# Optimization experiments

Hardware: AMD Instinct MI355X
Metric: run time of the kernel (lower is better)

The kernel has to match this reference:

```python
import jax, jax.numpy as jnp
import numpy as np

B, T, E = 32, 512, 256
H = 512          # num_cells
REV_H = 10       # hardcoded LSTM(10)
CONV_C = 60      # hardcoded Conv1D(60)
FEAT = 3 * CONV_C + REV_H  # 190
D0 = 100
TEMP = 1e-5
EPS = 1e-20


def setup_inputs() -> dict:
    key = jax.random.key(0)
    ks = jax.random.split(key, 18)
    def g(k, shape, fan_in):
        return (jax.random.normal(k, shape, jnp.float32) / np.float32(np.sqrt(fan_in)))
    inp = {}
    inp["x"] = jax.random.normal(ks[0], (B, T, E), jnp.float32)
    # Conv1D kernels in WIO layout [k, in, out]
    inp["conv1_w"] = g(ks[1], (3, E, CONV_C), 3 * E)
    inp["conv1_b"] = jnp.zeros((CONV_C,), jnp.float32)
    inp["conv2_w"] = g(ks[2], (4, E, CONV_C), 4 * E)
    inp["conv2_b"] = jnp.zeros((CONV_C,), jnp.float32)
    inp["conv3_w"] = g(ks[3], (5, E, CONV_C), 5 * E)
    inp["conv3_b"] = jnp.zeros((CONV_C,), jnp.float32)
    # reverse LSTM(10)
    inp["rev_Wx"] = g(ks[4], (E, 4 * REV_H), E)
    inp["rev_Wh"] = g(ks[5], (REV_H, 4 * REV_H), REV_H)
    inp["rev_b"] = jnp.zeros((4 * REV_H,), jnp.float32)
    # gate MLP: Dense(100, relu) -> Dense(2)
    inp["d0_W"] = g(ks[6], (FEAT + E, D0), FEAT + E)
    inp["d0_b"] = jnp.zeros((D0,), jnp.float32)
    inp["d1_W"] = g(ks[7], (D0, 2), D0)
    inp["d1_b"] = jnp.zeros((2,), jnp.float32)
    # main LSTMCell(H)
    inp["cell_Wx"] = g(ks[8], (E, 4 * H), E)
    inp["cell_Wh"] = g(ks[9], (H, 4 * H), H)
    inp["cell_b"] = jnp.zeros((4 * H,), jnp.float32)
    # pre-sampled Gumbel(0,1) noise, one per (t, b, 2)
    U = jax.random.uniform(ks[10], (T, B, 2), jnp.float32, 1e-7, 1.0)
    inp["gumbel_noise"] = -jnp.log(-jnp.log(U + EPS) + EPS)
    return inp


def _lstm_scan(xseq, Wx, Wh, b):
    # xseq: [T, B, E] -> hs: [T, B, H]
    h_dim = Wh.shape[0]
    bsz = xseq.shape[1]
    def step(carry, xt):
        h, c = carry
        z = xt @ Wx + h @ Wh + b
        i, f, g_, o = jnp.split(z, 4, axis=-1)
        c = jax.nn.sigmoid(f) * c + jax.nn.sigmoid(i) * jnp.tanh(g_)
        h = jax.nn.sigmoid(o) * jnp.tanh(c)
        return (h, c), h
    init = (jnp.zeros((bsz, h_dim), xseq.dtype), jnp.zeros((bsz, h_dim), xseq.dtype))
    _, hs = jax.lax.scan(step, init, xseq)
    return hs


def reference(x, conv1_w, conv1_b, conv2_w, conv2_b, conv3_w, conv3_b,
              rev_Wx, rev_Wh, rev_b, d0_W, d0_b, d1_W, d1_b,
              cell_Wx, cell_Wh, cell_b, gumbel_noise):
    dn = ('NWC', 'WIO', 'NWC')
    def conv(w, b_):
        return jax.lax.conv_general_dilated(x, w, (1,), 'SAME', dimension_numbers=dn) + b_
    conved = jnp.concatenate([conv(conv1_w, conv1_b), conv(conv2_w, conv2_b), conv(conv3_w, conv3_b)], axis=-1)  # [B,T,180]
    # LSTM over reversed sequence (output NOT re-reversed, as in the original)
    x_rev = x[:, ::-1, :].transpose(1, 0, 2)               # [T,B,E]
    rev = _lstm_scan(x_rev, rev_Wx, rev_Wh, rev_b).transpose(1, 0, 2)  # [B,T,10]
    f_core = jnp.concatenate([conved, rev], axis=-1)        # [B,T,190]
    # f_all[:, t+1] for t in [0,T): shift left by one, pad a zero row at the end
    ff_seq = jnp.concatenate([f_core[:, 1:, :], jnp.zeros_like(f_core[:, :1, :])], axis=1)  # [B,T,190]

    bsz = x.shape[0]
    h_dim = cell_Wh.shape[0]
    xs = (x.transpose(1, 0, 2), ff_seq.transpose(1, 0, 2), gumbel_noise)

    def step(carry, inputs):
        h, c = carry
        xt, ff, gn = inputs
        # skip-gate logits -> Gumbel-softmax (temperature 1e-5)
        hid = jax.nn.relu(jnp.concatenate([ff, xt], axis=-1) @ d0_W + d0_b)
        pi = hid @ d1_W + d1_b                               # [B,2]
        d = jax.nn.softmax((pi + gn) / TEMP, axis=-1)        # [B,2]
        # LSTM cell candidate
        z = xt @ cell_Wx + h @ cell_Wh + cell_b
        i, f, g_, o = jnp.split(z, 4, axis=-1)
        c_cand = jax.nn.sigmoid(f) * c + jax.nn.sigmoid(i) * jnp.tanh(g_)
        h_cand = jax.nn.sigmoid(o) * jnp.tanh(c_cand)
        d0, d1 = d[:, :1], d[:, 1:]
        h_new = d0 * h_cand + d1 * h
        c_new = d0 * c_cand + d1 * c
        # output written each step is the (ungated) candidate h, per the source
        return (h_new, c_new), h_cand

    init = (jnp.zeros((bsz, h_dim), x.dtype), jnp.zeros((bsz, h_dim), x.dtype))
    _, outs = jax.lax.scan(step, init, xs)                  # [T,B,H]
    return outs.transpose(1, 0, 2)                          # [B,T,H]
```

## Files before the change

kernel.cpp:

```cpp
#include <hip/hip_runtime.h>
#include <math.h>

#define Bz 32
#define Tz 512
#define Ez 256
#define Hz 512
#define FCH 446

__device__ __forceinline__ float sigf(float x){ return 1.0f/(1.0f + __expf(-x)); }
__device__ __forceinline__ float tanhfast(float x){ return 1.0f - 2.0f/(__expf(2.0f*x) + 1.0f); }

__global__ __launch_bounds__(256) void k_transpose_wh(const float* __restrict__ Wh, float* __restrict__ WhT){
  int idx = blockIdx.x*256 + threadIdx.x;
  int k = idx >> 11, c = idx & 2047;
  WhT[c*512 + k] = Wh[idx];
}

__global__ __launch_bounds__(256) void k_conv(
    const float* __restrict__ x,
    const float* __restrict__ w1, const float* __restrict__ b1,
    const float* __restrict__ w2, const float* __restrict__ b2,
    const float* __restrict__ w3, const float* __restrict__ b3,
    const float* __restrict__ rwx,
    float* __restrict__ feat, float* __restrict__ rxw)
{
  __shared__ __align__(16) float xs[256*40];
  int b  = blockIdx.x >> 4;
  int t0 = (blockIdx.x & 15) * 32;
  int tid = threadIdx.x;
  for (int i = 0; i < 36; ++i){
    int t = t0 - 2 + i;
    xs[tid*40 + i] = (t >= 0 && t < Tz) ? x[(b*Tz + t)*Ez + tid] : 0.0f;
  }
  __syncthreads();
  for (int i = 0; i < 32; ++i){
    int t = t0 + i;
    feat[((size_t)t*Bz + b)*FCH + 190 + tid] = xs[tid*40 + i + 2];
  }
  int tq = tid & 7, cs = tid >> 3;
  float acc[6][4];
  float racc[2][4];
  #pragma unroll
  for (int ci = 0; ci < 6; ++ci){
    int c = cs + 32*ci;
    float bv = 0.0f;
    if (c < 60) bv = b1[c];
    else if (c < 120) bv = b2[c-60];
    else if (c < 180) bv = b3[c-120];
    acc[ci][0]=acc[ci][1]=acc[ci][2]=acc[ci][3]=bv;
  }
  #pragma unroll
  for (int ji = 0; ji < 2; ++ji){ racc[ji][0]=racc[ji][1]=racc[ji][2]=racc[ji][3]=0.0f; }

  for (int e = 0; e < 256; ++e){
    const float* xr = &xs[e*40 + 4*tq];
    float4 wa = *(const float4*)(xr);
    float4 wb = *(const float4*)(xr + 4);
    float wd[8] = {wa.x, wa.y, wa.z, wa.w, wb.x, wb.y, wb.z, wb.w};
    #pragma unroll
    for (int ci = 0; ci < 6; ++ci){
      int c = cs + 32*ci;
      if (c < 60){
        #pragma unroll
        for (int k = 0; k < 3; ++k){
          float wv = w1[(k*256 + e)*60 + c];
          #pragma unroll
          for (int j = 0; j < 4; ++j) acc[ci][j] = fmaf(wd[1 + j + k], wv, acc[ci][j]);
        }
      } else if (c < 120){
        int cc = c - 60;
        #pragma unroll
        for (int k = 0; k < 4; ++k){
          float wv = w2[(k*256 + e)*60 + cc];
          #pragma unroll
          for (int j = 0; j < 4; ++j) acc[ci][j] = fmaf(wd[1 + j + k], wv, acc[ci][j]);
        }
      } else if (c < 180){
        int cc = c - 120;
        #pragma unroll
        for (int k = 0; k < 5; ++k){
          float wv = w3[(k*256 + e)*60 + cc];
          #pragma unroll
          for (int j = 0; j < 4; ++j) acc[ci][j] = fmaf(wd[j + k], wv, acc[ci][j]);
        }
      }
    }
    #pragma unroll
    for (int ji = 0; ji < 2; ++ji){
      int jc = cs + 32*ji;
      if (jc < 40){
        float wv = rwx[e*40 + jc];
        #pragma unroll
        for (int j = 0; j < 4; ++j) racc[ji][j] = fmaf(wd[2 + j], wv, racc[ji][j]);
      }
    }
  }
  #pragma unroll
  for (int ci = 0; ci < 6; ++ci){
    int c = cs + 32*ci;
    if (c < 180){
      #pragma unroll
      for (int j = 0; j < 4; ++j){
        int t = t0 + 4*tq + j;
        if (t >= 1) feat[((size_t)(t-1)*Bz + b)*FCH + c] = acc[ci][j];
      }
    }
  }
  #pragma unroll
  for (int ji = 0; ji < 2; ++ji){
    int jc = cs + 32*ji;
    if (jc < 40){
      #pragma unroll
      for (int j = 0; j < 4; ++j){
        int t = t0 + 4*tq + j;
        rxw[((size_t)(511 - t)*Bz + b)*40 + jc] = racc[ji][j];
      }
    }
  }
}

__global__ __launch_bounds__(64) void k_rev(const float* __restrict__ rxw,
    const float* __restrict__ revWh, const float* __restrict__ revb, float* __restrict__ feat){
  int b = blockIdx.x;
  int j = threadIdx.x;
  float wreg[10];
  float bias = 0.0f;
  #pragma unroll
  for (int k = 0; k < 10; ++k) wreg[k] = 0.0f;
  if (j < 40){
    bias = revb[j];
    #pragma unroll
    for (int k = 0; k < 10; ++k) wreg[k] = revWh[k*40 + j];
  }
  float h[10];
  #pragma unroll
  for (int k = 0; k < 10; ++k) h[k] = 0.0f;
  float c = 0.0f;
  for (int s = 0; s < Tz; ++s){
    float z = bias + ((j < 40) ? rxw[(s*Bz + b)*40 + j] : 0.0f);
    #pragma unroll
    for (int k = 0; k < 10; ++k) z = fmaf(h[k], wreg[k], z);
    float a = (j >= 20 && j < 30) ? tanhfast(z) : sigf(z);
    float af = __shfl(a, j + 10);
    float ag = __shfl(a, j + 20);
    float ao = __shfl(a, j + 30);
    if (j < 10) c = af*c + a*ag;
    float hn = ao * tanhfast(c);
    #pragma unroll
    for (int k = 0; k < 10; ++k) h[k] = __shfl(hn, k);
    if (j < 10 && s >= 1) feat[((size_t)(s-1)*Bz + b)*FCH + 180 + j] = hn;
  }
}

__global__ __launch_bounds__(256) void k_hid(const float* __restrict__ feat,
    const float* __restrict__ d0W, const float* __restrict__ d0b, float* __restrict__ hid){
  __shared__ __align__(16) float fT[446*36];
  int r0 = blockIdx.x * 32;
  int tid = threadIdx.x;
  for (int r = 0; r < 32; ++r){
    fT[tid*36 + r] = feat[(size_t)(r0 + r)*FCH + tid];
    if (tid < 190) fT[(tid + 256)*36 + r] = feat[(size_t)(r0 + r)*FCH + tid + 256];
  }
  __syncthreads();
  int cs = tid & 31, rq = tid >> 5;
  if (cs < 25){
    float4 accv[4];
    #pragma unroll
    for (int jc = 0; jc < 4; ++jc) accv[jc] = make_float4(0.f,0.f,0.f,0.f);
    for (int k = 0; k < 446; ++k){
      float4 xv = *(const float4*)&fT[k*36 + 4*rq];
      float4 wv = *(const float4*)&d0W[k*100 + 4*cs];
      accv[0].x = fmaf(xv.x, wv.x, accv[0].x); accv[0].y = fmaf(xv.y, wv.x, accv[0].y);
      accv[0].z = fmaf(xv.z, wv.x, accv[0].z); accv[0].w = fmaf(xv.w, wv.x, accv[0].w);
      accv[1].x = fmaf(xv.x, wv.y, accv[1].x); accv[1].y = fmaf(xv.y, wv.y, accv[1].y);
      accv[1].z = fmaf(xv.z, wv.y, accv[1].z); accv[1].w = fmaf(xv.w, wv.y, accv[1].w);
      accv[2].x = fmaf(xv.x, wv.z, accv[2].x); accv[2].y = fmaf(xv.y, wv.z, accv[2].y);
      accv[2].z = fmaf(xv.z, wv.z, accv[2].z); accv[2].w = fmaf(xv.w, wv.z, accv[2].w);
      accv[3].x = fmaf(xv.x, wv.w, accv[3].x); accv[3].y = fmaf(xv.y, wv.w, accv[3].y);
      accv[3].z = fmaf(xv.z, wv.w, accv[3].z); accv[3].w = fmaf(xv.w, wv.w, accv[3].w);
    }
    #pragma unroll
    for (int i = 0; i < 4; ++i){
      int row = r0 + 4*rq + i;
      float4 o;
      float vi[4] = { i==0?accv[0].x:(i==1?accv[0].y:(i==2?accv[0].z:accv[0].w)),
                      i==0?accv[1].x:(i==1?accv[1].y:(i==2?accv[1].z:accv[1].w)),
                      i==0?accv[2].x:(i==1?accv[2].y:(i==2?accv[2].z:accv[2].w)),
                      i==0?accv[3].x:(i==1?accv[3].y:(i==2?accv[3].z:accv[3].w)) };
      o.x = fmaxf(vi[0] + d0b[4*cs+0], 0.0f);
      o.y = fmaxf(vi[1] + d0b[4*cs+1], 0.0f);
      o.z = fmaxf(vi[2] + d0b[4*cs+2], 0.0f);
      o.w = fmaxf(vi[3] + d0b[4*cs+3], 0.0f);
      *(float4*)&hid[(size_t)row*100 + 4*cs] = o;
    }
  }
}

__global__ __launch_bounds__(128) void k_pi(const float* __restrict__ hid,
    const float* __restrict__ d1W, const float* __restrict__ d1b,
    const float* __restrict__ gum, float* __restrict__ d0a, float* __restrict__ d1a){
  __shared__ float hidL[64*100];
  int r0 = blockIdx.x * 64;
  int tid = threadIdx.x;
  for (int i = 0; i < 50; ++i) hidL[tid + 128*i] = hid[(size_t)r0*100 + tid + 128*i];
  __syncthreads();
  int r = tid >> 1, pp = tid & 1;
  float s = d1b[pp];
  for (int m = 0; m < 100; ++m) s = fmaf(hidL[r*100 + m], d1W[m*2 + pp], s);
  int row = r0 + r;
  float a = (s + gum[row*2 + pp]) / 1e-5f;
  float other = __shfl_xor(a, 1);
  float mx = fmaxf(a, other);
  float ea = expf(a - mx), eb = expf(other - mx);
  float d = ea / (ea + eb);
  if (pp == 0) d0a[row] = d; else d1a[row] = d;
}

__global__ __launch_bounds__(256) void k_xz(const float* __restrict__ x,
    const float* __restrict__ Wx, const float* __restrict__ cb, float* __restrict__ xzG){
  __shared__ __align__(16) float xT[256*36];
  int t  = blockIdx.x & 511;
  int c0 = (blockIdx.x >> 9) * 128;
  int tid = threadIdx.x;
  for (int b = 0; b < 32; ++b){
    xT[tid*36 + b] = x[(b*Tz + t)*Ez + tid];
  }
  __syncthreads();
  int cs = tid & 31, rq = tid >> 5;
  float4 accv[4];
  #pragma unroll
  for (int jc = 0; jc < 4; ++jc) accv[jc] = make_float4(0.f,0.f,0.f,0.f);
  for (int e = 0; e < 256; ++e){
    float4 xv = *(const float4*)&xT[e*36 + 4*rq];
    float4 wv = *(const float4*)&Wx[e*2048 + c0 + 4*cs];
    accv[0].x = fmaf(xv.x, wv.x, accv[0].x); accv[0].y = fmaf(xv.y, wv.x, accv[0].y);
    accv[0].z = fmaf(xv.z, wv.x, accv[0].z); accv[0].w = fmaf(xv.w, wv.x, accv[0].w);
    accv[1].x = fmaf(xv.x, wv.y, accv[1].x); accv[1].y = fmaf(xv.y, wv.y, accv[1].y);
    accv[1].z = fmaf(xv.z, wv.y, accv[1].z); accv[1].w = fmaf(xv.w, wv.y, accv[1].w);
    accv[2].x = fmaf(xv.x, wv.z, accv[2].x); accv[2].y = fmaf(xv.y, wv.z, accv[2].y);
    accv[2].z = fmaf(xv.z, wv.z, accv[2].z); accv[2].w = fmaf(xv.w, wv.z, accv[2].w);
    accv[3].x = fmaf(xv.x, wv.w, accv[3].x); accv[3].y = fmaf(xv.y, wv.w, accv[3].y);
    accv[3].z = fmaf(xv.z, wv.w, accv[3].z); accv[3].w = fmaf(xv.w, wv.w, accv[3].w);
  }
  #pragma unroll
  for (int jc = 0; jc < 4; ++jc){
    int col = c0 + 4*cs + jc;
    float bv = cb[col];
    float4 o = accv[jc];
    o.x += bv; o.y += bv; o.z += bv; o.w += bv;
    *(float4*)&xzG[(((size_t)rq*Tz + t)*2048 + col)*4] = o;
  }
}

__global__ __launch_bounds__(1024, 1) void k_scan(
    const float* __restrict__ WhT, const float* __restrict__ xzG,
    const float* __restrict__ d0a, const float* __restrict__ d1a,
    float* __restrict__ hG,
    unsigned int* __restrict__ barc,
    float* __restrict__ out)
{
  __shared__ __align__(16) float part[64*260];
  __shared__ __align__(16) float hL[4*520];
  __shared__ float zL[256];
  __shared__ float hcandL[64];

  int tid = threadIdx.x;
  int g = blockIdx.x & 7;
  int m = blockIdx.x >> 3;

  int cq = tid & 15;
  int kseg = tid >> 4;

  float wreg[4][8];
  #pragma unroll
  for (int ciq = 0; ciq < 4; ++ciq){
    int c = 4*cq + ciq;
    int col = ((c >> 4) << 9) + (m << 4) + (c & 15);
    const float4* wp = (const float4*)(WhT + (size_t)col*512 + kseg*8);
    float4 a = wp[0], bq = wp[1];
    wreg[ciq][0]=a.x;  wreg[ciq][1]=a.y;  wreg[ciq][2]=a.z;  wreg[ciq][3]=a.w;
    wreg[ciq][4]=bq.x; wreg[ciq][5]=bq.y; wreg[ciq][6]=bq.z; wreg[ciq][7]=bq.w;
  }

  int rc = tid >> 2, rb = tid & 3;
  int rcol = ((rc >> 4) << 9) + (m << 4) + (rc & 15);
  size_t xzbase = ((size_t)g*Tz)*8192 + (size_t)rcol*4 + rb;

  unsigned int* cnt = barc + g*64;
  float* hg0 = hG + (size_t)(g*2 + 0) * (4*512);
  float* hg1 = hG + (size_t)(g*2 + 1) * (4*512);

  float c_reg = 0.0f;

  for (int t = 0; t < Tz; ++t){
    const float* hcur = (t & 1) ? hg1 : hg0;
    float*       hnxt = (t & 1) ? hg0 : hg1;

    if (t == 0){
      int i0 = tid, i1 = tid + 1024;
      hL[(i0 >> 9)*520 + (i0 & 511)] = 0.0f;
      hL[(i1 >> 9)*520 + (i1 & 511)] = 0.0f;
    } else {
      int i0 = tid, i1 = tid + 1024;
      float v0 = __hip_atomic_load(hcur + i0, __ATOMIC_RELAXED, __HIP_MEMORY_SCOPE_AGENT);
      float v1 = __hip_atomic_load(hcur + i1, __ATOMIC_RELAXED, __HIP_MEMORY_SCOPE_AGENT);
      hL[(i0 >> 9)*520 + (i0 & 511)] = v0;
      hL[(i1 >> 9)*520 + (i1 & 511)] = v1;
    }
    float xzv = 0.0f;
    if (tid < 256) xzv = xzG[xzbase + (size_t)t*8192];
    float dv0 = 0.0f, dv1 = 0.0f;
    if (tid < 64){
      dv0 = d0a[t*32 + ((g << 2) + (tid & 3))];
      dv1 = d1a[t*32 + ((g << 2) + (tid & 3))];
    }
    __syncthreads();

    float acc[4][4];
    #pragma unroll
    for (int ciq = 0; ciq < 4; ++ciq)
      #pragma unroll
      for (int b = 0; b < 4; ++b) acc[ciq][b] = 0.0f;
    #pragma unroll
    for (int b = 0; b < 4; ++b){
      const float4* hp = (const float4*)&hL[b*520 + kseg*8];
      float4 h0 = hp[0], h1 = hp[1];
      float hv[8] = {h0.x,h0.y,h0.z,h0.w,h1.x,h1.y,h1.z,h1.w};
      #pragma unroll
      for (int j = 0; j < 8; ++j){
        #pragma unroll
        for (int ciq = 0; ciq < 4; ++ciq)
          acc[ciq][b] = fmaf(wreg[ciq][j], hv[j], acc[ciq][b]);
      }
    }
    {
      float* pw = &part[kseg*260 + 16*cq];
      *(float4*)(pw +  0) = make_float4(acc[0][0],acc[0][1],acc[0][2],acc[0][3]);
      *(float4*)(pw +  4) = make_float4(acc[1][0],acc[1][1],acc[1][2],acc[1][3]);
      *(float4*)(pw +  8) = make_float4(acc[2][0],acc[2][1],acc[2][2],acc[2][3]);
      *(float4*)(pw + 12) = make_float4(acc[3][0],acc[3][1],acc[3][2],acc[3][3]);
    }
    __syncthreads();

    if (tid < 256){
      float s0 = 0.f, s1 = 0.f, s2 = 0.f, s3 = 0.f;
      #pragma unroll
      for (int s = 0; s < 64; s += 4){
        s0 += part[(s+0)*260 + tid];
        s1 += part[(s+1)*260 + tid];
        s2 += part[(s+2)*260 + tid];
        s3 += part[(s+3)*260 + tid];
      }
      zL[tid] = (s0+s1)+(s2+s3) + xzv;
    }
    __syncthreads();

    if (tid < 64){
      int jl = tid >> 2, bb = tid & 3;
      float zi = zL[bb + 4*jl];
      float zf = zL[bb + 4*jl + 64];
      float zg = zL[bb + 4*jl + 128];
      float zo = zL[bb + 4*jl + 192];
      float hold = hL[bb*520 + (m << 4) + jl];
      float ccand = sigf(zf)*c_reg + sigf(zi)*tanhfast(zg);
      float hcand = sigf(zo)*tanhfast(ccand);
      c_reg = dv0*ccand + dv1*c_reg;
      float hnew = dv0*hcand + dv1*hold;
      hcandL[bb*16 + jl] = hcand;
      __hip_atomic_store(hnxt + bb*512 + (m << 4) + jl, hnew,
                         __ATOMIC_RELAXED, __HIP_MEMORY_SCOPE_AGENT);
    }
    __syncthreads();

    if (tid >= 64 && tid < 80){
      int idx = tid - 64; int bb = idx >> 2, q = idx & 3;
      float4 v = *(const float4*)&hcandL[bb*16 + 4*q];
      *(float4*)(out + (size_t)((g << 2) + bb)*(Tz*Hz) + (size_t)t*Hz + (m << 4) + 4*q) = v;
    }
    if (t < Tz-1){
      if (tid == 0){
        __hip_atomic_fetch_add(cnt, 1u, __ATOMIC_RELAXED, __HIP_MEMORY_SCOPE_AGENT);
        unsigned int target = 32u*(unsigned)(t+1);
        while (__hip_atomic_load(cnt, __ATOMIC_RELAXED, __HIP_MEMORY_SCOPE_AGENT) < target)
          __builtin_amdgcn_s_sleep(1);
      }
      __syncthreads();
    }
  }
}

extern "C" void kernel_launch(void* const* d_in, const int* in_sizes, int n_in,
                              void* d_out, int out_size, void* d_ws, size_t ws_size,
                              hipStream_t stream)
{
  const float* x       = (const float*)d_in[0];
  const float* conv1_w = (const float*)d_in[1];
  const float* conv1_b = (const float*)d_in[2];
  const float* conv2_w = (const float*)d_in[3];
  const float* conv2_b = (const float*)d_in[4];
  const float* conv3_w = (const float*)d_in[5];
  const float* conv3_b = (const float*)d_in[6];
  const float* rev_Wx  = (const float*)d_in[7];
  const float* rev_Wh  = (const float*)d_in[8];
  const float* rev_b   = (const float*)d_in[9];
  const float* d0_W    = (const float*)d_in[10];
  const float* d0_b    = (const float*)d_in[11];
  const float* d1_W    = (const float*)d_in[12];
  const float* d1_b    = (const float*)d_in[13];
  const float* cell_Wx = (const float*)d_in[14];
  const float* cell_Wh = (const float*)d_in[15];
  const float* cell_b  = (const float*)d_in[16];
  const float* gumbel  = (const float*)d_in[17];
  float* out = (float*)d_out;

  char* ws = (char*)d_ws;
  size_t off = 0;
  float* xzG  = (float*)(ws + off); off += (size_t)Tz*2048*Bz*4;
  float* feat = (float*)(ws + off); off += (size_t)Tz*Bz*FCH*4;
  float* WhT  = (float*)(ws + off); off += (size_t)Hz*2048*4;
  float* rxw  = (float*)(ws + off); off += (size_t)Tz*Bz*40*4;
  float* hid  = (float*)(ws + off); off += (size_t)Tz*Bz*100*4;
  float* d0a  = (float*)(ws + off); off += (size_t)Tz*Bz*4;
  float* d1a  = (float*)(ws + off); off += (size_t)Tz*Bz*4;
  float* hG   = (float*)(ws + off); off += (size_t)8*2*4*512*4;
  unsigned int* barc = (unsigned int*)(ws + off); off += 8*64*4;

  hipMemsetAsync(feat + (size_t)(Tz-1)*Bz*FCH, 0, Bz*FCH*4, stream);
  hipMemsetAsync(barc, 0, 8*64*4, stream);

  k_transpose_wh<<<4096, 256, 0, stream>>>(cell_Wh, WhT);
  k_conv<<<512, 256, 0, stream>>>(x, conv1_w, conv1_b, conv2_w, conv2_b,
                                  conv3_w, conv3_b, rev_Wx, feat, rxw);
  k_rev<<<32, 64, 0, stream>>>(rxw, rev_Wh, rev_b, feat);
  k_hid<<<512, 256, 0, stream>>>(feat, d0_W, d0_b, hid);
  k_pi<<<256, 128, 0, stream>>>(hid, d1_W, d1_b, gumbel, d0a, d1a);
  k_xz<<<8192, 256, 0, stream>>>(x, cell_Wx, cell_b, xzG);

  k_scan<<<256, 1024, 0, stream>>>(WhT, xzG, d0a, d1a, hG, barc, out);
}
```

Baseline: 3.062 ms.

## Shrink scan blocks to 512 threads with shuffle-based butterfly reduction

The recurrent scan kernel now uses 512 threads per block. Each thread holds 8 weight columns across 8 k-values, and the partial sums are reduced with a three-stage xor-shuffle butterfly inside each wavefront, so the shared-memory partial buffer drops from 64 rows to 8. The h-vector staging uses float4 stores with an XOR swizzle to avoid bank conflicts. The k_xz kernel also prefetches the next weight row into registers for software pipelining. The gain is less shared-memory traffic and shorter reductions on the serial critical path, at the cost of more registers per thread (64 weights plus 32 accumulators).

```diff
diff --git a/kernel.cpp b/kernel.cpp
--- a/kernel.cpp
+++ b/kernel.cpp
@@ -230,17 +230,19 @@
   float4 accv[4];
   #pragma unroll
   for (int jc = 0; jc < 4; ++jc) accv[jc] = make_float4(0.f,0.f,0.f,0.f);
+  float4 wv = *(const float4*)&Wx[c0 + 4*cs];
   for (int e = 0; e < 256; ++e){
+    float4 wc = wv;
+    if (e != 255) wv = *(const float4*)&Wx[(e+1)*2048 + c0 + 4*cs];
     float4 xv = *(const float4*)&xT[e*36 + 4*rq];
-    float4 wv = *(const float4*)&Wx[e*2048 + c0 + 4*cs];
-    accv[0].x = fmaf(xv.x, wv.x, accv[0].x); accv[0].y = fmaf(xv.y, wv.x, accv[0].y);
-    accv[0].z = fmaf(xv.z, wv.x, accv[0].z); accv[0].w = fmaf(xv.w, wv.x, accv[0].w);
-    accv[1].x = fmaf(xv.x, wv.y, accv[1].x); accv[1].y = fmaf(xv.y, wv.y, accv[1].y);
-    accv[1].z = fmaf(xv.z, wv.y, accv[1].z); accv[1].w = fmaf(xv.w, wv.y, accv[1].w);
-    accv[2].x = fmaf(xv.x, wv.z, accv[2].x); accv[2].y = fmaf(xv.y, wv.z, accv[2].y);
-    accv[2].z = fmaf(xv.z, wv.z, accv[2].z); accv[2].w = fmaf(xv.w, wv.z, accv[2].w);
-    accv[3].x = fmaf(xv.x, wv.w, accv[3].x); accv[3].y = fmaf(xv.y, wv.w, accv[3].y);
-    accv[3].z = fmaf(xv.z, wv.w, accv[3].z); accv[3].w = fmaf(xv.w, wv.w, accv[3].w);
+    accv[0].x = fmaf(xv.x, wc.x, accv[0].x); accv[0].y = fmaf(xv.y, wc.x, accv[0].y);
+    accv[0].z = fmaf(xv.z, wc.x, accv[0].z); accv[0].w = fmaf(xv.w, wc.x, accv[0].w);
+    accv[1].x = fmaf(xv.x, wc.y, accv[1].x); accv[1].y = fmaf(xv.y, wc.y, accv[1].y);
+    accv[1].z = fmaf(xv.z, wc.y, accv[1].z); accv[1].w = fmaf(xv.w, wc.y, accv[1].w);
+    accv[2].x = fmaf(xv.x, wc.z, accv[2].x); accv[2].y = fmaf(xv.y, wc.z, accv[2].y);
+    accv[2].z = fmaf(xv.z, wc.z, accv[2].z); accv[2].w = fmaf(xv.w, wc.z, accv[2].w);
+    accv[3].x = fmaf(xv.x, wc.w, accv[3].x); accv[3].y = fmaf(xv.y, wc.w, accv[3].y);
+    accv[3].z = fmaf(xv.z, wc.w, accv[3].z); accv[3].w = fmaf(xv.w, wc.w, accv[3].w);
   }
   #pragma unroll
   for (int jc = 0; jc < 4; ++jc){
@@ -252,38 +254,46 @@
   }
 }
 
-__global__ __launch_bounds__(1024, 1) void k_scan(
+__global__ __launch_bounds__(512, 2) void k_scan(
     const float* __restrict__ WhT, const float* __restrict__ xzG,
     const float* __restrict__ d0a, const float* __restrict__ d1a,
     float* __restrict__ hG,
     unsigned int* __restrict__ barc,
     float* __restrict__ out)
 {
-  __shared__ __align__(16) float part[64*260];
   __shared__ __align__(16) float hL[4*520];
+  __shared__ __align__(16) float part[8*260];
   __shared__ float zL[256];
   __shared__ float hcandL[64];
 
   int tid = threadIdx.x;
   int g = blockIdx.x & 7;
   int m = blockIdx.x >> 3;
-
-  int cq = tid & 15;
-  int kseg = tid >> 4;
-
-  float wreg[4][8];
-  #pragma unroll
-  for (int ciq = 0; ciq < 4; ++ciq){
-    int c = 4*cq + ciq;
+  int w = tid >> 6;
+  int lane = tid & 63;
+
+  float wreg[8][8];
+  #pragma unroll
+  for (int ci = 0; ci < 8; ++ci){
+    int c = 8*w + ci;
     int col = ((c >> 4) << 9) + (m << 4) + (c & 15);
-    const float4* wp = (const float4*)(WhT + (size_t)col*512 + kseg*8);
+    const float4* wp = (const float4*)(WhT + (size_t)col*512 + lane*8);
     float4 a = wp[0], bq = wp[1];
-    wreg[ciq][0]=a.x;  wreg[ciq][1]=a.y;  wreg[ciq][2]=a.z;  wreg[ciq][3]=a.w;
-    wreg[ciq][4]=bq.x; wreg[ciq][5]=bq.y; wreg[ciq][6]=bq.z; wreg[ciq][7]=bq.w;
-  }
-
-  int rc = tid >> 2, rb = tid & 3;
-  int rcol = ((rc >> 4) << 9) + (m << 4) + (rc & 15);
+    wreg[ci][0]=a.x;  wreg[ci][1]=a.y;  wreg[ci][2]=a.z;  wreg[ci][3]=a.w;
+    wreg[ci][4]=bq.x; wreg[ci][5]=bq.y; wreg[ci][6]=bq.z; wreg[ci][7]=bq.w;
+  }
+
+  int q0 = 2*lane;
+  int sw = (q0 >> 3) & 3;
+  int p0 = ((q0  ) ^ sw) << 2;
+  int p1 = ((q0+1) ^ sw) << 2;
+
+  int stb = tid >> 7, stq = tid & 127;
+  int stp = (stq ^ ((stq >> 3) & 3)) << 2;
+  const int hrow = 520;
+
+  int rcg = tid >> 2, rb = tid & 3;
+  int rcol = ((rcg >> 4) << 9) + (m << 4) + (rcg & 15);
   size_t xzbase = ((size_t)g*Tz)*8192 + (size_t)rcol*4 + rb;
 
   unsigned int* cnt = barc + g*64;
@@ -297,15 +307,15 @@
     float*       hnxt = (t & 1) ? hg0 : hg1;
 
     if (t == 0){
-      int i0 = tid, i1 = tid + 1024;
-      hL[(i0 >> 9)*520 + (i0 & 511)] = 0.0f;
-      hL[(i1 >> 9)*520 + (i1 & 511)] = 0.0f;
+      *(float4*)&hL[stb*hrow + stp] = make_float4(0.f,0.f,0.f,0.f);
     } else {
-      int i0 = tid, i1 = tid + 1024;
-      float v0 = __hip_atomic_load(hcur + i0, __ATOMIC_RELAXED, __HIP_MEMORY_SCOPE_AGENT);
-      float v1 = __hip_atomic_load(hcur + i1, __ATOMIC_RELAXED, __HIP_MEMORY_SCOPE_AGENT);
-      hL[(i0 >> 9)*520 + (i0 & 511)] = v0;
-      hL[(i1 >> 9)*520 + (i1 & 511)] = v1;
+      const float* src = hcur + stb*512 + stq*4;
+      float4 v;
+      v.x = __hip_atomic_load(src+0, __ATOMIC_RELAXED, __HIP_MEMORY_SCOPE_AGENT);
+      v.y = __hip_atomic_load(src+1, __ATOMIC_RELAXED, __HIP_MEMORY_SCOPE_AGENT);
+      v.z = __hip_atomic_load(src+2, __ATOMIC_RELAXED, __HIP_MEMORY_SCOPE_AGENT);
+      v.w = __hip_atomic_load(src+3, __ATOMIC_RELAXED, __HIP_MEMORY_SCOPE_AGENT);
+      *(float4*)&hL[stb*hrow + stp] = v;
     }
     float xzv = 0.0f;
     if (tid < 256) xzv = xzG[xzbase + (size_t)t*8192];
@@ -316,65 +326,95 @@
     }
     __syncthreads();
 
-    float acc[4][4];
-    #pragma unroll
-    for (int ciq = 0; ciq < 4; ++ciq)
-      #pragma unroll
-      for (int b = 0; b < 4; ++b) acc[ciq][b] = 0.0f;
+    float acc[8][4];
+    #pragma unroll
+    for (int ci = 0; ci < 8; ++ci)
+      #pragma unroll
+      for (int b = 0; b < 4; ++b) acc[ci][b] = 0.0f;
     #pragma unroll
     for (int b = 0; b < 4; ++b){
-      const float4* hp = (const float4*)&hL[b*520 + kseg*8];
-      float4 h0 = hp[0], h1 = hp[1];
+      const float* hr = &hL[b*hrow];
+      float4 h0 = *(const float4*)(hr + p0);
+      float4 h1 = *(const float4*)(hr + p1);
       float hv[8] = {h0.x,h0.y,h0.z,h0.w,h1.x,h1.y,h1.z,h1.w};
       #pragma unroll
       for (int j = 0; j < 8; ++j){
         #pragma unroll
-        for (int ciq = 0; ciq < 4; ++ciq)
-          acc[ciq][b] = fmaf(wreg[ciq][j], hv[j], acc[ciq][b]);
-      }
-    }
+        for (int ci = 0; ci < 8; ++ci)
+          acc[ci][b] = fmaf(wreg[ci][j], hv[j], acc[ci][b]);
+      }
+    }
+
+    float v16[16];
     {
-      float* pw = &part[kseg*260 + 16*cq];
-      *(float4*)(pw +  0) = make_float4(acc[0][0],acc[0][1],acc[0][2],acc[0][3]);
-      *(float4*)(pw +  4) = make_float4(acc[1][0],acc[1][1],acc[1][2],acc[1][3]);
-      *(float4*)(pw +  8) = make_float4(acc[2][0],acc[2][1],acc[2][2],acc[2][3]);
-      *(float4*)(pw + 12) = make_float4(acc[3][0],acc[3][1],acc[3][2],acc[3][3]);
+      bool hi = (lane & 1);
+      #pragma unroll
+      for (int i = 0; i < 16; ++i){
+        int ci = i >> 2, b = i & 3;
+        float keep = hi ? acc[4+ci][b] : acc[ci][b];
+        float send = hi ? acc[ci][b]   : acc[4+ci][b];
+        v16[i] = keep + __shfl_xor(send, 1);
+      }
+    }
+    float v8[8];
+    {
+      bool hi = (lane & 2);
+      #pragma unroll
+      for (int i = 0; i < 8; ++i){
+        float keep = hi ? v16[8+i] : v16[i];
+        float send = hi ? v16[i]   : v16[8+i];
+        v8[i] = keep + __shfl_xor(send, 2);
+      }
+    }
+    float v4[4];
+    {
+      bool hi = (lane & 4);
+      #pragma unroll
+      for (int b = 0; b < 4; ++b){
+        float keep = hi ? v8[4+b] : v8[b];
+        float send = hi ? v8[b]   : v8[4+b];
+        v4[b] = keep + __shfl_xor(send, 4);
+      }
+    }
+    {
+      int e = ((lane & 1) << 2) | (lane & 2) | ((lane >> 2) & 1);
+      float* pw = &part[(lane >> 3)*260 + ((8*w + e) << 2)];
+      *(float4*)pw = make_float4(v4[0], v4[1], v4[2], v4[3]);
     }
     __syncthreads();
 
     if (tid < 256){
-      float s0 = 0.f, s1 = 0.f, s2 = 0.f, s3 = 0.f;
-      #pragma unroll
-      for (int s = 0; s < 64; s += 4){
-        s0 += part[(s+0)*260 + tid];
-        s1 += part[(s+1)*260 + tid];
-        s2 += part[(s+2)*260 + tid];
-        s3 += part[(s+3)*260 + tid];
-      }
+      float s0 = part[0*260 + tid] + part[1*260 + tid];
+      float s1 = part[2*260 + tid] + part[3*260 + tid];
+      float s2 = part[4*260 + tid] + part[5*260 + tid];
+      float s3 = part[6*260 + tid] + part[7*260 + tid];
       zL[tid] = (s0+s1)+(s2+s3) + xzv;
     }
     __syncthreads();
 
     if (tid < 64){
       int jl = tid >> 2, bb = tid & 3;
-      float zi = zL[bb + 4*jl];
-      float zf = zL[bb + 4*jl + 64];
-      float zg = zL[bb + 4*jl + 128];
-      float zo = zL[bb + 4*jl + 192];
-      float hold = hL[bb*520 + (m << 4) + jl];
+      float zi = zL[      (jl << 2) + bb];
+      float zf = zL[ 64 + (jl << 2) + bb];
+      float zg = zL[128 + (jl << 2) + bb];
+      float zo = zL[192 + (jl << 2) + bb];
+      int hk = (m << 4) + jl;
+      int hq = hk >> 2;
+      int hph = (hq ^ ((hq >> 3) & 3)) << 2;
+      float hold = hL[bb*hrow + hph + (hk & 3)];
       float ccand = sigf(zf)*c_reg + sigf(zi)*tanhfast(zg);
       float hcand = sigf(zo)*tanhfast(ccand);
       c_reg = dv0*ccand + dv1*c_reg;
       float hnew = dv0*hcand + dv1*hold;
-      hcandL[bb*16 + jl] = hcand;
-      __hip_atomic_store(hnxt + bb*512 + (m << 4) + jl, hnew,
+      hcandL[(bb << 4) + jl] = hcand;
+      __hip_atomic_store(hnxt + bb*512 + hk, hnew,
                          __ATOMIC_RELAXED, __HIP_MEMORY_SCOPE_AGENT);
     }
     __syncthreads();
 
     if (tid >= 64 && tid < 80){
       int idx = tid - 64; int bb = idx >> 2, q = idx & 3;
-      float4 v = *(const float4*)&hcandL[bb*16 + 4*q];
+      float4 v = *(const float4*)&hcandL[(bb << 4) + 4*q];
       *(float4*)(out + (size_t)((g << 2) + bb)*(Tz*Hz) + (size_t)t*Hz + (m << 4) + 4*q) = v;
     }
     if (t < Tz-1){
@@ -436,5 +476,5 @@
   k_pi<<<256, 128, 0, stream>>>(hid, d1_W, d1_b, gumbel, d0a, d1a);
   k_xz<<<8192, 256, 0, stream>>>(x, cell_Wx, cell_b, xzG);
 
-  k_scan<<<256, 1024, 0, stream>>>(WhT, xzG, d0a, d1a, hG, barc, out);
-}
+  k_scan<<<256, 512, 0, stream>>>(WhT, xzG, d0a, d1a, hG, barc, out);
+}
```

Result: slower. 3.164 ms (+3.3%).
